# Optimization experiments

Measured on AMD Instinct MI355X. Metric: run time of the kernel, lower is better.

## Reference

```python
import jax, jax.numpy as jnp
import numpy as np
import math

D_MODEL = 2048
N_HEADS = 16
D_HEAD = D_MODEL // N_HEADS
MAX_T = 2048
B, T = 2, 2048


def rotate_half(x):
    # interleaved rotate: (x0,x1,x2,x3,...) -> (-x1,x0,-x3,x2,...)
    x1 = x[..., ::2]
    x2 = x[..., 1::2]
    return jnp.stack((-x2, x1), axis=-1).reshape(x.shape)


def setup_inputs() -> dict:
    key = jax.random.key(0)
    k1, k2, k3 = jax.random.split(key, 3)
    x = jax.random.normal(k1, (B, T, D_MODEL), dtype=jnp.float32)
    # torch nn.Linear weights: [out, in]
    s = 1.0 / math.sqrt(D_MODEL)
    Wqkv = jax.random.uniform(k2, (3 * D_MODEL, D_MODEL), dtype=jnp.float32, minval=-s, maxval=s)
    WO = jax.random.uniform(k3, (D_MODEL, D_MODEL), dtype=jnp.float32, minval=-s, maxval=s)
    return {"x": x, "Wqkv": Wqkv, "WO": WO}


def reference(x, Wqkv, WO):
    Bx, Tx, _ = x.shape
    # RoPE tables (buffers)
    pos = jnp.arange(Tx, dtype=jnp.float32)
    freqs = jnp.exp(-math.log(10000.0) * jnp.arange(0, D_HEAD, 2, dtype=jnp.float32) / D_HEAD)
    angles = pos[:, None] * freqs[None, :]               # [T, d_head/2]
    sin = jnp.repeat(jnp.sin(angles), 2, axis=-1)        # [T, d_head]
    cos = jnp.repeat(jnp.cos(angles), 2, axis=-1)
    sin = sin[None, None, :, :]
    cos = cos[None, None, :, :]

    qkv = x @ Wqkv.T                                     # [B, T, 3D]
    q, k, v = jnp.split(qkv, 3, axis=-1)
    def to_heads(t):
        return t.reshape(Bx, Tx, N_HEADS, D_HEAD).transpose(0, 2, 1, 3)  # [B,H,T,d]
    q, k, v = to_heads(q), to_heads(k), to_heads(v)

    q = q * cos + rotate_half(q) * sin
    k = k * cos + rotate_half(k) * sin

    scores = jnp.einsum('bhqd,bhkd->bhqk', q, k) / math.sqrt(D_HEAD)
    mask = jnp.triu(jnp.full((Tx, Tx), -jnp.inf, dtype=scores.dtype), k=1)
    scores = scores + mask
    attn = jax.nn.softmax(scores, axis=-1)
    out = jnp.einsum('bhqk,bhkd->bhqd', attn, v)
    out = out.transpose(0, 2, 1, 3).reshape(Bx, Tx, D_MODEL)
    return out @ WO.T
```

## Files before the change

kernel.cpp:

```cpp
#include <hip/hip_runtime.h>
#include <hip/hip_bf16.h>

typedef unsigned short u16;
typedef __attribute__((ext_vector_type(8))) short bf16x8;
typedef __attribute__((ext_vector_type(4))) float f32x4;

#define B_   2
#define T_   2048
#define DM   2048
#define NH   16
#define DH   128
#define NQKV 6144

__device__ __forceinline__ u16 f2bf(float f) {
  __hip_bfloat16 h = __float2bfloat16(f);
  u16 u; __builtin_memcpy(&u, &h, 2); return u;
}
__device__ __forceinline__ float bf2f(u16 u) {
  __hip_bfloat16 h; __builtin_memcpy(&h, &u, 2); return __bfloat162float(h);
}
__device__ __forceinline__ void gl_lds16(const void* g, void* l) {
  __builtin_amdgcn_global_load_lds(
      (__attribute__((address_space(1))) unsigned int*)g,
      (__attribute__((address_space(3))) unsigned int*)l, 16, 0, 0);
}
__device__ __forceinline__ f32x4 MFMA(bf16x8 a, bf16x8 b, f32x4 c) {
  return __builtin_amdgcn_mfma_f32_16x16x32_bf16(a, b, c, 0, 0, 0);
}

__global__ __launch_bounds__(256) void cast_kernel(const float* __restrict__ in,
                                                   u16* __restrict__ out, int n4) {
  int i = blockIdx.x * 256 + threadIdx.x;
  if (i >= n4) return;
  float4 v = ((const float4*)in)[i];
  ushort4 o;
  o.x = f2bf(v.x); o.y = f2bf(v.y); o.z = f2bf(v.z); o.w = f2bf(v.w);
  ((ushort4*)out)[i] = o;
}

#define G1_M 4096
#define G1_N 6144
#define G1_K 2048

#define MFMA_Q(AQ, M0)                                                        \
  _Pragma("unroll") for (int e_ = 0; e_ < 2; ++e_)                            \
  _Pragma("unroll") for (int n_ = 0; n_ < 4; ++n_)                            \
  _Pragma("unroll") for (int kb_ = 0; kb_ < 2; ++kb_)                         \
    acc[(M0) + e_][n_] = MFMA(AQ[e_][kb_], bfr[n_][kb_], acc[(M0) + e_][n_])

#define BARRIER() asm volatile("s_barrier" ::: "memory")
#define LGKM0()                                                               \
  do {                                                                        \
    asm volatile("s_waitcnt lgkmcnt(0)" ::: "memory");                        \
    __builtin_amdgcn_sched_barrier(0);                                        \
  } while (0)
#define SBAR() __builtin_amdgcn_sched_barrier(0)

__global__ __launch_bounds__(512, 2) void gemm1_8ph(const u16* __restrict__ A,
                                                    const u16* __restrict__ Bm,
                                                    u16* __restrict__ C) {
  __shared__ alignas(16) u16 As[2][256 * 64];
  __shared__ alignas(16) u16 Bs[2][256 * 64];
  const int tid = threadIdx.x;
  const int w = tid >> 6, lane = tid & 63;
  const int lrow = lane & 15, quad = lane >> 4;
  const long tileM = (long)blockIdx.y * 256, tileN = (long)blockIdx.x * 256;
  const int wm = (w >> 2) * 128, wn = (w & 3) * 64;

  const int sw8 = w * 8;
  const int srowL = lane >> 3;
  const int schunk = ((lane & 7) ^ srowL) * 8;
  const u16* Ag0 = A + (tileM + sw8 + srowL) * (long)G1_K + schunk;
  const u16* Bg0 = Bm + (tileN + sw8 + srowL) * (long)G1_K + schunk;

  auto stgA = [&](int tt, int h) {
    const int b = tt & 1;
    gl_lds16(Ag0 + (size_t)(h * 128) * G1_K + tt * 64,
             &As[b][(h * 128 + sw8) * 64]);
    gl_lds16(Ag0 + (size_t)(h * 128 + 64) * G1_K + tt * 64,
             &As[b][(h * 128 + 64 + sw8) * 64]);
  };
  auto stgB = [&](int tt, int h) {
    const int b = tt & 1;
    gl_lds16(Bg0 + (size_t)(h * 128) * G1_K + tt * 64,
             &Bs[b][(h * 128 + sw8) * 64]);
    gl_lds16(Bg0 + (size_t)(h * 128 + 64) * G1_K + tt * 64,
             &Bs[b][(h * 128 + 64 + sw8) * 64]);
  };

  const int aBase = (wm + lrow) * 64;
  const int bBase = (wn + lrow) * 64;
  const int slot[2] = { (quad ^ (lrow & 7)) * 8, ((4 + quad) ^ (lrow & 7)) * 8 };

  f32x4 acc[8][4] = {};
  bf16x8 bfr[4][2];
  bf16x8 aCur[2][2], aNxt[2][2];

  stgA(0, 0); stgA(0, 1); stgB(0, 0); stgB(0, 1);
  stgB(1, 0); stgB(1, 1); stgA(1, 0);
  asm volatile("s_waitcnt vmcnt(6)" ::: "memory");
  BARRIER();
#pragma unroll
  for (int ni = 0; ni < 4; ++ni)
#pragma unroll
    for (int kb = 0; kb < 2; ++kb)
      bfr[ni][kb] = *(const bf16x8*)(Bs[0] + bBase + ni * 1024 + slot[kb]);
#pragma unroll
  for (int e = 0; e < 2; ++e)
#pragma unroll
    for (int kb = 0; kb < 2; ++kb)
      aCur[e][kb] = *(const bf16x8*)(As[0] + aBase + e * 1024 + slot[kb]);

#pragma unroll 1
  for (int t = 0; t < 32; ++t) {
    const u16* AsC = As[t & 1];
    LGKM0();
    __builtin_amdgcn_s_setprio(1);
    MFMA_Q(aCur, 0);
    __builtin_amdgcn_s_setprio(0);
    SBAR();
#pragma unroll
    for (int e = 0; e < 2; ++e)
#pragma unroll
      for (int kb = 0; kb < 2; ++kb)
        aNxt[e][kb] = *(const bf16x8*)(AsC + aBase + (2 + e) * 1024 + slot[kb]);
    if (t + 1 < 32) stgA(t + 1, 1);
    BARRIER();
    LGKM0();
    __builtin_amdgcn_s_setprio(1);
    MFMA_Q(aNxt, 2);
    __builtin_amdgcn_s_setprio(0);
    SBAR();
#pragma unroll
    for (int e = 0; e < 2; ++e)
#pragma unroll
      for (int kb = 0; kb < 2; ++kb)
        aCur[e][kb] = *(const bf16x8*)(AsC + aBase + (4 + e) * 1024 + slot[kb]);
    if (t + 2 < 32) stgB(t + 2, 0);
    BARRIER();
    LGKM0();
    __builtin_amdgcn_s_setprio(1);
    MFMA_Q(aCur, 4);
    __builtin_amdgcn_s_setprio(0);
    SBAR();
#pragma unroll
    for (int e = 0; e < 2; ++e)
#pragma unroll
      for (int kb = 0; kb < 2; ++kb)
        aNxt[e][kb] = *(const bf16x8*)(AsC + aBase + (6 + e) * 1024 + slot[kb]);
    if (t + 2 < 32) stgB(t + 2, 1);
    if (t < 30) { asm volatile("s_waitcnt vmcnt(4)" ::: "memory"); }
    else       { asm volatile("s_waitcnt vmcnt(0)" ::: "memory"); }
    BARRIER();
    LGKM0();
    __builtin_amdgcn_s_setprio(1);
    MFMA_Q(aNxt, 6);
    __builtin_amdgcn_s_setprio(0);
    SBAR();
    if (t + 1 < 32) {
      const u16* AsN = As[(t + 1) & 1];
      const u16* BsN = Bs[(t + 1) & 1];
#pragma unroll
      for (int ni = 0; ni < 4; ++ni)
#pragma unroll
        for (int kb = 0; kb < 2; ++kb)
          bfr[ni][kb] = *(const bf16x8*)(BsN + bBase + ni * 1024 + slot[kb]);
#pragma unroll
      for (int e = 0; e < 2; ++e)
#pragma unroll
        for (int kb = 0; kb < 2; ++kb)
          aCur[e][kb] = *(const bf16x8*)(AsN + aBase + e * 1024 + slot[kb]);
    }
    if (t + 2 < 32) stgA(t + 2, 0);
    BARRIER();
  }

  const long crow = tileM + wm + quad * 4;
  const long ccol = tileN + wn + lrow;
#pragma unroll
  for (int mi = 0; mi < 8; ++mi)
#pragma unroll
    for (int ni = 0; ni < 4; ++ni)
#pragma unroll
      for (int r = 0; r < 4; ++r)
        C[(crow + mi * 16 + r) * (long)G1_N + (ccol + ni * 16)] =
            f2bf(acc[mi][ni][r]);
}

__global__ __launch_bounds__(256) void gemm_bt(const u16* __restrict__ A,
                                               const u16* __restrict__ Bm,
                                               void* __restrict__ Cp,
                                               int M, int N, int K, int out_f32) {
  __shared__ u16 As[128 * 64];
  __shared__ u16 Bs[128 * 64];
  const int tid  = threadIdx.x;
  const int wave = tid >> 6, lane = tid & 63;
  const int lrow = lane & 15, quad = lane >> 4;
  const long tileM = (long)blockIdx.y * 128, tileN = (long)blockIdx.x * 128;
  const int wm = (wave >> 1) * 64, wn = (wave & 1) * 64;
  const int sRowIn = lane >> 3;
  const int sChunk = (lane & 7) ^ sRowIn;
  const int sRow0  = wave * 32 + sRowIn;
  const u16* Ag = A + (tileM + sRow0) * (long)K + sChunk * 8;
  const u16* Bg = Bm + (tileN + sRow0) * (long)K + sChunk * 8;
  u16* AsW = As + wave * 2048;
  u16* BsW = Bs + wave * 2048;
  f32x4 acc[4][4] = {};
  for (int kt = 0; kt < K; kt += 64) {
#pragma unroll
    for (int i = 0; i < 4; ++i)
      gl_lds16(Ag + kt + (size_t)i * 8 * K, AsW + i * 512);
#pragma unroll
    for (int i = 0; i < 4; ++i)
      gl_lds16(Bg + kt + (size_t)i * 8 * K, BsW + i * 512);
    __syncthreads();
#pragma unroll
    for (int kb = 0; kb < 2; ++kb) {
      const int slot8 = (((kb * 4 + quad) ^ (lrow & 7)) * 8);
      bf16x8 af[4], bfr[4];
#pragma unroll
      for (int i = 0; i < 4; ++i)
        af[i]  = *(const bf16x8*)(As + (wm + i * 16 + lrow) * 64 + slot8);
#pragma unroll
      for (int i = 0; i < 4; ++i)
        bfr[i] = *(const bf16x8*)(Bs + (wn + i * 16 + lrow) * 64 + slot8);
#pragma unroll
      for (int mi = 0; mi < 4; ++mi)
#pragma unroll
        for (int ni = 0; ni < 4; ++ni)
          acc[mi][ni] = MFMA(af[mi], bfr[ni], acc[mi][ni]);
    }
    __syncthreads();
  }
  const long crow = tileM + wm + quad * 4;
  const long ccol = tileN + wn + lrow;
  if (out_f32) {
    float* C = (float*)Cp;
#pragma unroll
    for (int mi = 0; mi < 4; ++mi)
#pragma unroll
      for (int ni = 0; ni < 4; ++ni)
#pragma unroll
        for (int r = 0; r < 4; ++r)
          C[(crow + mi * 16 + r) * (long)N + (ccol + ni * 16)] = acc[mi][ni][r];
  } else {
    u16* C = (u16*)Cp;
#pragma unroll
    for (int mi = 0; mi < 4; ++mi)
#pragma unroll
      for (int ni = 0; ni < 4; ++ni)
#pragma unroll
        for (int r = 0; r < 4; ++r)
          C[(crow + mi * 16 + r) * (long)N + (ccol + ni * 16)] = f2bf(acc[mi][ni][r]);
  }
}

__global__ __launch_bounds__(256) void rope_reorder(const u16* __restrict__ qkv,
                                                    u16* __restrict__ Q,
                                                    u16* __restrict__ Kd,
                                                    u16* __restrict__ Vt) {
  const int tt = blockIdx.x;
  const int bh = blockIdx.y;
  const int b = bh >> 4, h = bh & 15;
  const int tid = threadIdx.x;
  __shared__ u16 vlds[64 * 129];
  const float qscale = 0.08838834764831845f;
#pragma unroll
  for (int it = 0; it < 16; ++it) {
    int p  = tid + it * 256;
    int tl = p >> 6;
    int i  = p & 63;
    int t  = tt * 64 + tl;
    float freq  = __expf(-9.210340371976184f * (float)i / 64.0f);
    float angle = (float)t * freq;
    float sn, cs;
    sincosf(angle, &sn, &cs);
    const u16* row = qkv + (size_t)(b * T_ + t) * NQKV;
    size_t qo = ((size_t)bh * T_ + t) * DH + 2 * i;
    float q0 = bf2f(row[h * DH + 2 * i]), q1 = bf2f(row[h * DH + 2 * i + 1]);
    Q[qo]     = f2bf((q0 * cs - q1 * sn) * qscale);
    Q[qo + 1] = f2bf((q1 * cs + q0 * sn) * qscale);
    float k0 = bf2f(row[DM + h * DH + 2 * i]), k1 = bf2f(row[DM + h * DH + 2 * i + 1]);
    Kd[qo]     = f2bf(k0 * cs - k1 * sn);
    Kd[qo + 1] = f2bf(k1 * cs + k0 * sn);
  }
#pragma unroll
  for (int it = 0; it < 32; ++it) {
    int idx = tid + it * 256;
    int tl = idx >> 7, d = idx & 127;
    vlds[tl * 129 + d] =
        qkv[(size_t)(b * T_ + tt * 64 + tl) * NQKV + 2 * DM + h * DH + d];
  }
  __syncthreads();
#pragma unroll
  for (int it = 0; it < 32; ++it) {
    int idx = tid + it * 256;
    int d = idx >> 6, tl = idx & 63;
    Vt[((size_t)bh * DH + d) * T_ + tt * 64 + tl] = vlds[tl * 129 + d];
  }
}

__global__ __launch_bounds__(256) void attn_flash(const u16* __restrict__ Q,
                                                  const u16* __restrict__ K,
                                                  const u16* __restrict__ Vt,
                                                  u16* __restrict__ AO) {
  __shared__ u16 Kl[64 * 128];
  __shared__ u16 Vl[128 * 64];
  __shared__ u16 Pl[4 * 16 * 64];
  const int pairIdx = blockIdx.x;
  const int bh = blockIdx.y;
  const int b = bh >> 4, h = bh & 15;
  const int tid = threadIdx.x;
  const int wave = tid >> 6, lane = tid & 63;
  const int lrow = lane & 15, quad = lane >> 4;
  const u16* Qb = Q + (size_t)bh * T_ * DH;
  const u16* Kb = K + (size_t)bh * T_ * DH;
  const u16* Vb = Vt + (size_t)bh * DH * T_;

  u16* KlW = Kl + wave * 2048;
  u16* VlW = Vl + wave * 2048;
  const int kRowIn = lane >> 4;
  const int vRowIn = lane >> 3;
  const int vChunk = (lane & 7) ^ vRowIn;
  u16* PlW = Pl + wave * 1024;

  for (int pass = 0; pass < 2; ++pass) {
    const int qt = pass == 0 ? (2 * gridDim.x - 1 - pairIdx) : pairIdx;
    const int qbase = qt * 64;

    bf16x8 qf[4];
    {
      const u16* qrow = Qb + (size_t)(qbase + wave * 16 + lrow) * DH + quad * 8;
#pragma unroll
      for (int kc = 0; kc < 4; ++kc) qf[kc] = *(const bf16x8*)(qrow + kc * 32);
    }
    f32x4 o[8] = {};
    float lsum[4] = {0.f, 0.f, 0.f, 0.f};

    for (int j = 0; j <= qt; ++j) {
#pragma unroll
      for (int i = 0; i < 4; ++i) {
        int krow = wave * 16 + i * 4 + kRowIn;
        int kch = (lane & 15) ^ (i * 4 + kRowIn);
        gl_lds16(Kb + (size_t)(j * 64 + krow) * DH + kch * 8, KlW + i * 512);
      }
#pragma unroll
      for (int i = 0; i < 4; ++i) {
        int vd = wave * 32 + i * 8 + vRowIn;
        gl_lds16(Vb + (size_t)vd * T_ + j * 64 + vChunk * 8, VlW + i * 512);
      }
      __syncthreads();

      f32x4 s[4] = {};
#pragma unroll
      for (int kc = 0; kc < 4; ++kc)
#pragma unroll
        for (int ns = 0; ns < 4; ++ns) {
          bf16x8 kf = *(const bf16x8*)(Kl + (ns * 16 + lrow) * 128 +
                                       (((kc * 4 + quad) ^ lrow) * 8));
          s[ns] = MFMA(qf[kc], kf, s[ns]);
        }
      if (j == qt) {
#pragma unroll
        for (int ns = 0; ns < 4; ++ns)
#pragma unroll
          for (int r = 0; r < 4; ++r)
            if (ns * 16 + lrow > wave * 16 + quad * 4 + r) s[ns][r] = -__builtin_inff();
      }
#pragma unroll
      for (int r = 0; r < 4; ++r) {
        const int prow = quad * 4 + r;
#pragma unroll
        for (int ns = 0; ns < 4; ++ns) {
          float p = __expf(s[ns][r]);
          PlW[prow * 64 + (((ns * 2 + (lrow >> 3)) ^ (prow & 7)) * 8) +
              (lrow & 7)] = f2bf(p);
          lsum[r] += p;
        }
      }

#pragma unroll
      for (int kc = 0; kc < 2; ++kc) {
        bf16x8 pf = *(const bf16x8*)(PlW + lrow * 64 +
                                     (((kc * 4 + quad) ^ (lrow & 7)) * 8));
#pragma unroll
        for (int os = 0; os < 8; ++os) {
          bf16x8 vf = *(const bf16x8*)(Vl + (os * 16 + lrow) * 64 +
                                       (((kc * 4 + quad) ^ (lrow & 7)) * 8));
          o[os] = MFMA(pf, vf, o[os]);
        }
      }
      __syncthreads();
    }
#pragma unroll
    for (int r = 0; r < 4; ++r) {
      lsum[r] += __shfl_xor(lsum[r], 1, 16);
      lsum[r] += __shfl_xor(lsum[r], 2, 16);
      lsum[r] += __shfl_xor(lsum[r], 4, 16);
      lsum[r] += __shfl_xor(lsum[r], 8, 16);
    }
#pragma unroll
    for (int r = 0; r < 4; ++r) {
      float inv = 1.0f / lsum[r];
      const size_t row = (size_t)b * T_ + qbase + wave * 16 + quad * 4 + r;
      u16* dst = AO + row * DM + h * DH;
#pragma unroll
      for (int os = 0; os < 8; ++os) dst[os * 16 + lrow] = f2bf(o[os][r] * inv);
    }
  }
}

extern "C" void kernel_launch(void* const* d_in, const int* in_sizes, int n_in,
                              void* d_out, int out_size, void* d_ws, size_t ws_size,
                              hipStream_t stream) {
  const float* x    = (const float*)d_in[0];
  const float* Wqkv = (const float*)d_in[1];
  const float* WO   = (const float*)d_in[2];
  char* ws = (char*)d_ws;
  size_t off = 0;
  u16* xb   = (u16*)(ws + off); off += (size_t)B_ * T_ * DM * 2;
  u16* wqb  = (u16*)(ws + off); off += (size_t)NQKV * DM * 2;
  u16* wob  = (u16*)(ws + off); off += (size_t)DM * DM * 2;
  u16* qkvb = (u16*)(ws + off); off += (size_t)B_ * T_ * NQKV * 2;
  u16* Qb   = (u16*)(ws + off); off += (size_t)B_ * NH * T_ * DH * 2;
  u16* Kb   = (u16*)(ws + off); off += (size_t)B_ * NH * T_ * DH * 2;
  u16* Vtb  = (u16*)(ws + off); off += (size_t)B_ * NH * T_ * DH * 2;
  u16* AO   = xb;

  cast_kernel<<<(B_ * T_ * DM / 4 + 255) / 256, 256, 0, stream>>>(x, xb, B_ * T_ * DM / 4);
  cast_kernel<<<(NQKV * DM / 4 + 255) / 256, 256, 0, stream>>>(Wqkv, wqb, NQKV * DM / 4);
  cast_kernel<<<(DM * DM / 4 + 255) / 256, 256, 0, stream>>>(WO, wob, DM * DM / 4);

  gemm1_8ph<<<dim3(G1_N / 256, G1_M / 256), 512, 0, stream>>>(xb, wqb, qkvb);

  rope_reorder<<<dim3(T_ / 64, B_ * NH), 256, 0, stream>>>(qkvb, Qb, Kb, Vtb);

  attn_flash<<<dim3(T_ / 128, B_ * NH), 256, 0, stream>>>(Qb, Kb, Vtb, AO);

  gemm_bt<<<dim3(DM / 128, B_ * T_ / 128), 256, 0, stream>>>(
      AO, wob, d_out, B_ * T_, DM, DM, 1);
}
```

Before: 382.9 us.

## Fuse RoPE, scaling and head reorder into QKV GEMM epilogue

The QKV projection GEMM now writes Q and K directly in per-head layout with RoPE (and the softmax scale on Q) applied in its epilogue, using a lane shuffle to get the paired element. V is written transposed straight from the accumulators. This removes the separate rope_reorder kernel and the round trip of the full qkv intermediate through memory. In exchange the epilogue computes sincos per element, and its Q/K stores are scattered 2-byte writes that may be less coalesced.

New measurement: 442.7 us. 15.6% more time.

```diff
diff --git a/kernel.cpp b/kernel.cpp
--- a/kernel.cpp
+++ b/kernel.cpp
@@ -58,7 +58,9 @@
 
 __global__ __launch_bounds__(512, 2) void gemm1_8ph(const u16* __restrict__ A,
                                                     const u16* __restrict__ Bm,
-                                                    u16* __restrict__ C) {
+                                                    u16* __restrict__ Qo,
+                                                    u16* __restrict__ Ko,
+                                                    u16* __restrict__ Vt) {
   __shared__ alignas(16) u16 As[2][256 * 64];
   __shared__ alignas(16) u16 Bs[2][256 * 64];
   const int tid = threadIdx.x;
@@ -177,14 +179,51 @@
 
   const long crow = tileM + wm + quad * 4;
   const long ccol = tileN + wn + lrow;
-#pragma unroll
-  for (int mi = 0; mi < 8; ++mi)
-#pragma unroll
-    for (int ni = 0; ni < 4; ++ni)
-#pragma unroll
-      for (int r = 0; r < 4; ++r)
-        C[(crow + mi * 16 + r) * (long)G1_N + (ccol + ni * 16)] =
-            f2bf(acc[mi][ni][r]);
+  const int sec = (int)(tileN >> 11);
+  if (sec < 2) {
+    u16* dst = sec == 0 ? Qo : Ko;
+    const float scale = sec == 0 ? 0.08838834764831845f : 1.0f;
+#pragma unroll
+    for (int ni = 0; ni < 4; ++ni) {
+      const long col = ccol + ni * 16;
+      const int cws = (int)(col & 2047);
+      const int h = cws >> 7, d = cws & 127;
+      const int i = d >> 1;
+      const float freq = __expf(-9.210340371976184f * (float)i / 64.0f);
+#pragma unroll
+      for (int mi = 0; mi < 8; ++mi) {
+#pragma unroll
+        for (int r = 0; r < 4; ++r) {
+          const long row = crow + mi * 16 + r;
+          const int b = (int)(row >> 11), tt = (int)(row & 2047);
+          float x = acc[mi][ni][r];
+          float p = __shfl_xor(x, 1);
+          float sn, cs;
+          sincosf((float)tt * freq, &sn, &cs);
+          float o = (x * cs + ((d & 1) ? p : -p) * sn) * scale;
+          dst[(((size_t)(b * 16 + h)) * T_ + tt) * DH + d] = f2bf(o);
+        }
+      }
+    }
+  } else {
+#pragma unroll
+    for (int ni = 0; ni < 4; ++ni) {
+      const long col = ccol + ni * 16;
+      const int cws = (int)(col & 2047);
+      const int h = cws >> 7, d = cws & 127;
+#pragma unroll
+      for (int mi = 0; mi < 8; ++mi) {
+        const long row0 = crow + mi * 16;
+        const int b = (int)(row0 >> 11), t0 = (int)(row0 & 2047);
+        ushort4 v4;
+        v4.x = f2bf(acc[mi][ni][0]);
+        v4.y = f2bf(acc[mi][ni][1]);
+        v4.z = f2bf(acc[mi][ni][2]);
+        v4.w = f2bf(acc[mi][ni][3]);
+        *(ushort4*)(Vt + (((size_t)(b * 16 + h)) * DH + d) * (size_t)T_ + t0) = v4;
+      }
+    }
+  }
 }
 
 __global__ __launch_bounds__(256) void gemm_bt(const u16* __restrict__ A,
@@ -255,51 +294,6 @@
   }
 }
 
-__global__ __launch_bounds__(256) void rope_reorder(const u16* __restrict__ qkv,
-                                                    u16* __restrict__ Q,
-                                                    u16* __restrict__ Kd,
-                                                    u16* __restrict__ Vt) {
-  const int tt = blockIdx.x;
-  const int bh = blockIdx.y;
-  const int b = bh >> 4, h = bh & 15;
-  const int tid = threadIdx.x;
-  __shared__ u16 vlds[64 * 129];
-  const float qscale = 0.08838834764831845f;
-#pragma unroll
-  for (int it = 0; it < 16; ++it) {
-    int p  = tid + it * 256;
-    int tl = p >> 6;
-    int i  = p & 63;
-    int t  = tt * 64 + tl;
-    float freq  = __expf(-9.210340371976184f * (float)i / 64.0f);
-    float angle = (float)t * freq;
-    float sn, cs;
-    sincosf(angle, &sn, &cs);
-    const u16* row = qkv + (size_t)(b * T_ + t) * NQKV;
-    size_t qo = ((size_t)bh * T_ + t) * DH + 2 * i;
-    float q0 = bf2f(row[h * DH + 2 * i]), q1 = bf2f(row[h * DH + 2 * i + 1]);
-    Q[qo]     = f2bf((q0 * cs - q1 * sn) * qscale);
-    Q[qo + 1] = f2bf((q1 * cs + q0 * sn) * qscale);
-    float k0 = bf2f(row[DM + h * DH + 2 * i]), k1 = bf2f(row[DM + h * DH + 2 * i + 1]);
-    Kd[qo]     = f2bf(k0 * cs - k1 * sn);
-    Kd[qo + 1] = f2bf(k1 * cs + k0 * sn);
-  }
-#pragma unroll
-  for (int it = 0; it < 32; ++it) {
-    int idx = tid + it * 256;
-    int tl = idx >> 7, d = idx & 127;
-    vlds[tl * 129 + d] =
-        qkv[(size_t)(b * T_ + tt * 64 + tl) * NQKV + 2 * DM + h * DH + d];
-  }
-  __syncthreads();
-#pragma unroll
-  for (int it = 0; it < 32; ++it) {
-    int idx = tid + it * 256;
-    int d = idx >> 6, tl = idx & 63;
-    Vt[((size_t)bh * DH + d) * T_ + tt * 64 + tl] = vlds[tl * 129 + d];
-  }
-}
-
 __global__ __launch_bounds__(256) void attn_flash(const u16* __restrict__ Q,
                                                   const u16* __restrict__ K,
                                                   const u16* __restrict__ Vt,
@@ -421,7 +415,6 @@
   u16* xb   = (u16*)(ws + off); off += (size_t)B_ * T_ * DM * 2;
   u16* wqb  = (u16*)(ws + off); off += (size_t)NQKV * DM * 2;
   u16* wob  = (u16*)(ws + off); off += (size_t)DM * DM * 2;
-  u16* qkvb = (u16*)(ws + off); off += (size_t)B_ * T_ * NQKV * 2;
   u16* Qb   = (u16*)(ws + off); off += (size_t)B_ * NH * T_ * DH * 2;
   u16* Kb   = (u16*)(ws + off); off += (size_t)B_ * NH * T_ * DH * 2;
   u16* Vtb  = (u16*)(ws + off); off += (size_t)B_ * NH * T_ * DH * 2;
@@ -431,9 +424,7 @@
   cast_kernel<<<(NQKV * DM / 4 + 255) / 256, 256, 0, stream>>>(Wqkv, wqb, NQKV * DM / 4);
   cast_kernel<<<(DM * DM / 4 + 255) / 256, 256, 0, stream>>>(WO, wob, DM * DM / 4);
 
-  gemm1_8ph<<<dim3(G1_N / 256, G1_M / 256), 512, 0, stream>>>(xb, wqb, qkvb);
-
-  rope_reorder<<<dim3(T_ / 64, B_ * NH), 256, 0, stream>>>(qkvb, Qb, Kb, Vtb);
+  gemm1_8ph<<<dim3(G1_N / 256, G1_M / 256), 512, 0, stream>>>(xb, wqb, Qb, Kb, Vtb);
 
   attn_flash<<<dim3(T_ / 128, B_ * NH), 256, 0, stream>>>(Qb, Kb, Vtb, AO);
 
```
